# Kernel optimization log

Measured on AMD Instinct MI355X. Metric: run time of the kernel, lower is better.

Reference implementation:

```python
import jax, jax.numpy as jnp
import numpy as np

HEADS = 8
DIM_HEAD = 64
EPS = 1e-5  # nn.InstanceNorm1d default


def _inst_norm(t):
    # t: [b, h, n, d]; InstanceNorm1d(dim_head) on (b*h, n, d) input normalizes
    # over the last (L) axis per (instance, channel) = per (b, h, n) token.
    mu = jnp.mean(t, axis=-1, keepdims=True)
    var = jnp.var(t, axis=-1, keepdims=True)  # biased, matches torch eval-mode IN
    return (t - mu) / jnp.sqrt(var + EPS)


def setup_inputs() -> dict:
    key = jax.random.key(0)
    k1, k2, k3, k4 = jax.random.split(key, 4)
    b, n, dim = 4, 8192, 256
    inner = HEADS * DIM_HEAD  # 512
    x = jax.random.normal(k1, (b, n, dim), dtype=jnp.float32)
    w_qkv = jax.random.normal(k2, (dim, 3 * inner), dtype=jnp.float32) * (1.0 / DIM_HEAD)
    w_out = jax.random.normal(k3, (inner, dim), dtype=jnp.float32) * (dim ** -0.5)
    b_out = jax.random.normal(k4, (dim,), dtype=jnp.float32) * 0.01
    return {"x": x, "w_qkv": w_qkv, "w_out": w_out, "b_out": b_out}


def reference(x, w_qkv, w_out, b_out):
    b, n, dim = x.shape
    qkv = x @ w_qkv                                   # [b, n, 3*inner]
    q, k, v = jnp.split(qkv, 3, axis=-1)
    to_heads = lambda t: t.reshape(b, n, HEADS, DIM_HEAD).transpose(0, 2, 1, 3)  # b h n d
    q, k, v = to_heads(q), to_heads(k), to_heads(v)
    # Galerkin: instance-norm K and V
    k = _inst_norm(k)
    v = _inst_norm(v)
    # associative linear attention: (k^T v) then q @ dots, scaled by 1/n
    dots = jnp.einsum('bhnd,bhne->bhde', k, v)        # [b, h, d, d]
    out = jnp.einsum('bhnd,bhde->bhne', q, dots) * (1.0 / n)  # [b, h, n, d]
    out = out.transpose(0, 2, 1, 3).reshape(b, n, HEADS * DIM_HEAD)
    return out @ w_out + b_out                        # dropout p=0 (eval)
```

## Files before the change

kernel.cpp:

```cpp
#include <hip/hip_runtime.h>
#include <hip/hip_bf16.h>
#include <stdint.h>

#define HEADS 8
#define DHEAD 64
#define BATCH 4
#define SEQ   8192
#define DIM   256
#define INNER 512
#define QKVC  1536
#define ROWS  32768
#define EPS   1e-5f

typedef unsigned short u16;
typedef unsigned long long u64;
typedef __attribute__((ext_vector_type(8))) short bf16x8;
typedef __attribute__((ext_vector_type(4))) float f32x4;

#define AS1 __attribute__((address_space(1)))
#define AS3 __attribute__((address_space(3)))

__device__ __forceinline__ void async16(const void* g, void* l) {
  __builtin_amdgcn_global_load_lds((AS1 unsigned int*)g, (AS3 unsigned int*)l, 16, 0, 0);
}

__device__ __forceinline__ float bf2f(u16 u) {
  union { uint32_t i; float f; } v; v.i = ((uint32_t)u) << 16; return v.f;
}
__device__ __forceinline__ u16 f2bf(float f) {
  union { float f; uint32_t i; } v; v.f = f;
  uint32_t x = v.i;
  return (u16)((x + 0x7fffu + ((x >> 16) & 1u)) >> 16);
}

__global__ __launch_bounds__(256) void prep(const float* __restrict__ x,
                                            const float* __restrict__ w,
                                            u16* __restrict__ xb,
                                            u16* __restrict__ wqB,
                                            u16* __restrict__ wkvP,
                                            float* __restrict__ dots) {
  int bid = blockIdx.x;
  if (bid < 8192) {
    int i = (bid * 256 + threadIdx.x) * 4;
    float4 v = *(const float4*)(x + i);
    ushort4 o; o.x = f2bf(v.x); o.y = f2bf(v.y); o.z = f2bf(v.z); o.w = f2bf(v.w);
    *(ushort4*)(xb + i) = o;
  } else if (bid < 8704) {
    int id = (bid - 8192) * 256 + threadIdx.x;
    int k = id >> 9, j = id & 511;
    wqB[id] = f2bf(w[k * QKVC + j]);
  } else if (bid < 9728) {
    int id = (bid - 8704) * 256 + threadIdx.x;
    int j    = id & 7;
    int lane = (id >> 3) & 63;
    int frag = (id >> 9) & 63;
    int h    = id >> 15;
    int fn   = frag & 3;
    int half = (frag >> 2) & 1;
    int ks   = (frag >> 3) & 1;
    int kk   = frag >> 4;
    int col  = half * 64 + fn * 16 + (lane & 15);
    int kidx = kk * 64 + ks * 32 + (lane >> 4) * 8 + j;
    int oc   = (col < 64) ? (512 + h * 64 + col) : (1024 + h * 64 + (col - 64));
    wkvP[id] = f2bf(w[kidx * QKVC + oc]);
  } else {
    int i = ((bid - 9728) * 256 + threadIdx.x) * 4;
    float4 z; z.x = 0.f; z.y = 0.f; z.z = 0.f; z.w = 0.f;
    *(float4*)(dots + i) = z;
  }
}

__device__ __forceinline__ void gemm_tile(const u16* __restrict__ A, int lda,
                                          const u16* __restrict__ Bt, int ldb,
                                          int K, int row0, int col0,
                                          u16* sA, u16* sB, f32x4 acc[4][4]) {
  const int tid = threadIdx.x, lane = tid & 63, wave = tid >> 6;
  const int m = lane & 15, q = lane >> 4;
  const int mr = (wave >> 1) * 64, nc = (wave & 1) * 64;
  for (int kk = 0; kk < K; kk += 64) {
#pragma unroll
    for (int it = 0; it < 4; ++it) {
      int c = it * 256 + tid;
      int r = c >> 3, kc = (c ^ r) & 7;
      async16(A + (size_t)(row0 + r) * lda + kk + kc * 8, sA + (it * 256 + wave * 64) * 8);
      async16(Bt + (size_t)(col0 + r) * ldb + kk + kc * 8, sB + (it * 256 + wave * 64) * 8);
    }
    __syncthreads();
#pragma unroll
    for (int ks = 0; ks < 2; ++ks) {
      bf16x8 af[4], bfr[4];
#pragma unroll
      for (int f = 0; f < 4; ++f) {
        int ra = mr + f * 16 + m;
        int rb = nc + f * 16 + m;
        af[f]  = *(const bf16x8*)&sA[ra * 64 + (((ks * 4 + q) ^ (m & 7)) * 8)];
        bfr[f] = *(const bf16x8*)&sB[rb * 64 + (((ks * 4 + q) ^ (m & 7)) * 8)];
      }
#pragma unroll
      for (int fm = 0; fm < 4; ++fm)
#pragma unroll
        for (int fn = 0; fn < 4; ++fn)
          acc[fm][fn] = __builtin_amdgcn_mfma_f32_16x16x32_bf16(af[fm], bfr[fn], acc[fm][fn], 0, 0, 0);
    }
    __syncthreads();
  }
}

__global__ __launch_bounds__(256, 3) void gemm_kv_dots(const u16* __restrict__ A,
                                                       const u16* __restrict__ wkvP,
                                                       float* __restrict__ dots) {
  __shared__ alignas(16) u16 smem[17408];
  u16* sA  = smem;
  u16* knT = smem;
  u16* vnT = smem + 8704;

  const int tid = threadIdx.x, lane = tid & 63, wave = tid >> 6;
  const int m = lane & 15, q = lane >> 4;
  const int row0 = blockIdx.x * 128;
  const int h = blockIdx.y;
  const int half = wave & 1;
  const int rowbase = (wave >> 1) * 64;
  const u16* bp = wkvP + (size_t)h * 32768 + lane * 8;

  f32x4 acc[4][4];
#pragma unroll
  for (int i = 0; i < 4; ++i)
#pragma unroll
    for (int j = 0; j < 4; ++j) acc[i][j] = (f32x4){0.f, 0.f, 0.f, 0.f};

#pragma unroll
  for (int kk = 0; kk < 4; ++kk) {
    bf16x8 breg[2][4];
#pragma unroll
    for (int ks = 0; ks < 2; ++ks)
#pragma unroll
      for (int fn = 0; fn < 4; ++fn)
        breg[ks][fn] = *(const bf16x8*)(bp + (size_t)((((kk * 2 + ks) * 2 + half) * 4 + fn) * 512));
#pragma unroll
    for (int it = 0; it < 4; ++it) {
      int c = it * 256 + tid;
      int r = c >> 3, kc = (c ^ r) & 7;
      async16(A + (size_t)(row0 + r) * DIM + kk * 64 + kc * 8, sA + (it * 256 + wave * 64) * 8);
    }
    __syncthreads();
#pragma unroll
    for (int ks = 0; ks < 2; ++ks) {
      bf16x8 af[4];
#pragma unroll
      for (int f = 0; f < 4; ++f) {
        int r = rowbase + f * 16 + m;
        af[f] = *(const bf16x8*)&sA[r * 64 + (((ks * 4 + q) ^ (m & 7)) * 8)];
      }
#pragma unroll
      for (int fm = 0; fm < 4; ++fm)
#pragma unroll
        for (int fn = 0; fn < 4; ++fn)
          acc[fm][fn] = __builtin_amdgcn_mfma_f32_16x16x32_bf16(af[fm], breg[ks][fn], acc[fm][fn], 0, 0, 0);
    }
    __syncthreads();
  }

  u16* dst = half ? vnT : knT;
#pragma unroll
  for (int fm = 0; fm < 4; ++fm) {
    f32x4 s  = acc[fm][0] + acc[fm][1] + acc[fm][2] + acc[fm][3];
    f32x4 s2 = (f32x4){0.f, 0.f, 0.f, 0.f};
#pragma unroll
    for (int fn = 0; fn < 4; ++fn)
#pragma unroll
      for (int r = 0; r < 4; ++r) s2[r] = fmaf(acc[fm][fn][r], acc[fm][fn][r], s2[r]);
#pragma unroll
    for (int mask = 1; mask <= 8; mask <<= 1) {
#pragma unroll
      for (int r = 0; r < 4; ++r) {
        s[r]  += __shfl_xor(s[r],  mask, 64);
        s2[r] += __shfl_xor(s2[r], mask, 64);
      }
    }
    f32x4 mu, rs;
#pragma unroll
    for (int r = 0; r < 4; ++r) {
      mu[r] = s[r] * (1.f / 64.f);
      float var = s2[r] * (1.f / 64.f) - mu[r] * mu[r];
      rs[r] = rsqrtf(var + EPS);
    }
    const int tokb = rowbase + fm * 16 + q * 4;
#pragma unroll
    for (int fn = 0; fn < 4; ++fn) {
      int d = fn * 16 + m;
      u64 pk = 0;
#pragma unroll
      for (int r = 0; r < 4; ++r) {
        u16 hv = f2bf((acc[fm][fn][r] - mu[r]) * rs[r]);
        pk |= (u64)hv << (16 * r);
      }
      *(u64*)(dst + d * 136 + tokb) = pk;
    }
  }
  __syncthreads();

  f32x4 dacc[4];
#pragma unroll
  for (int f = 0; f < 4; ++f) dacc[f] = (f32x4){0.f, 0.f, 0.f, 0.f};
#pragma unroll
  for (int ks = 0; ks < 4; ++ks) {
    bf16x8 a = *(const bf16x8*)&knT[(wave * 16 + m) * 136 + ks * 32 + q * 8];
#pragma unroll
    for (int fn = 0; fn < 4; ++fn) {
      bf16x8 bb = *(const bf16x8*)&vnT[(fn * 16 + m) * 136 + ks * 32 + q * 8];
      dacc[fn] = __builtin_amdgcn_mfma_f32_16x16x32_bf16(a, bb, dacc[fn], 0, 0, 0);
    }
  }

  const int b = blockIdx.x >> 6;
  float* dbase = dots + (size_t)(b * 8 + h) * 4096;
#pragma unroll
  for (int fn = 0; fn < 4; ++fn) {
    int e = fn * 16 + m;
#pragma unroll
    for (int r = 0; r < 4; ++r) {
      int d = wave * 16 + q * 4 + r;
      atomicAdd(dbase + d * 64 + e, dacc[fn][r]);
    }
  }
}

__global__ __launch_bounds__(256) void make_M(const float* __restrict__ dots,
                                              const float* __restrict__ wout,
                                              u16* __restrict__ Mbt) {
  __shared__ float dl[8][64];
  const int bh = blockIdx.x, b = bh >> 3, h = bh & 7;
  const int jg = blockIdx.y;
  const int c = threadIdx.x;
  for (int i = threadIdx.x; i < 512; i += 256)
    ((float*)dl)[i] = dots[(size_t)bh * 4096 + jg * 512 + i];
  __syncthreads();
  float accv[8];
#pragma unroll
  for (int jj = 0; jj < 8; ++jj) accv[jj] = 0.f;
  for (int e = 0; e < 64; ++e) {
    float w = wout[(h * 64 + e) * DIM + c];
#pragma unroll
    for (int jj = 0; jj < 8; ++jj) accv[jj] = fmaf(dl[jj][e], w, accv[jj]);
  }
  const float inv_n = 1.0f / (float)SEQ;
  u16* outp = Mbt + ((size_t)(b * 256 + c)) * 512 + h * 64 + jg * 8;
#pragma unroll
  for (int jj = 0; jj < 8; ++jj) outp[jj] = f2bf(accv[jj] * inv_n);
}

__global__ __launch_bounds__(256) void make_G(const u16* __restrict__ Mbt,
                                              const u16* __restrict__ wqB,
                                              u16* __restrict__ Gt) {
  __shared__ alignas(16) u16 sA[128 * 64];
  __shared__ alignas(16) u16 sB[128 * 64];
  const int lane = threadIdx.x & 63, wave = threadIdx.x >> 6;
  const int row0 = blockIdx.x * 128, col0 = blockIdx.y * 128;
  const int b = blockIdx.z;
  f32x4 acc[4][4];
#pragma unroll
  for (int i = 0; i < 4; ++i)
#pragma unroll
    for (int j = 0; j < 4; ++j) acc[i][j] = (f32x4){0.f, 0.f, 0.f, 0.f};

  gemm_tile(Mbt + (size_t)b * 256 * 512, INNER, wqB, INNER, INNER, row0, col0, sA, sB, acc);

  u16* out = Gt + (size_t)b * 256 * 256;
  const int mr = (wave >> 1) * 64, nc = (wave & 1) * 64;
#pragma unroll
  for (int fm = 0; fm < 4; ++fm) {
    int rbase = row0 + mr + fm * 16 + (lane >> 4) * 4;
#pragma unroll
    for (int fn = 0; fn < 4; ++fn) {
      int col = col0 + nc + fn * 16 + (lane & 15);
#pragma unroll
      for (int r = 0; r < 4; ++r)
        out[(size_t)(rbase + r) * DIM + col] = f2bf(acc[fm][fn][r]);
    }
  }
}

__global__ __launch_bounds__(256) void gemm_out(const u16* __restrict__ A,
                                                const u16* __restrict__ Gt,
                                                const float* __restrict__ bias,
                                                float* __restrict__ out) {
  __shared__ alignas(16) u16 sA[128 * 64];
  __shared__ alignas(16) u16 sB[128 * 64];
  const int lane = threadIdx.x & 63, wave = threadIdx.x >> 6;
  const int row0 = blockIdx.x * 128, col0 = blockIdx.y * 128;
  const int b = blockIdx.x >> 6;
  const u16* Bt = Gt + (size_t)b * 256 * 256;
  f32x4 acc[4][4];
#pragma unroll
  for (int i = 0; i < 4; ++i)
#pragma unroll
    for (int j = 0; j < 4; ++j) acc[i][j] = (f32x4){0.f, 0.f, 0.f, 0.f};

  gemm_tile(A, DIM, Bt, DIM, DIM, row0, col0, sA, sB, acc);

  const int mr = (wave >> 1) * 64, nc = (wave & 1) * 64;
#pragma unroll
  for (int fm = 0; fm < 4; ++fm) {
    int rbase = row0 + mr + fm * 16 + (lane >> 4) * 4;
#pragma unroll
    for (int fn = 0; fn < 4; ++fn) {
      int col = col0 + nc + fn * 16 + (lane & 15);
      float bb = bias[col];
#pragma unroll
      for (int r = 0; r < 4; ++r)
        out[(size_t)(rbase + r) * DIM + col] = acc[fm][fn][r] + bb;
    }
  }
}

extern "C" void kernel_launch(void* const* d_in, const int* in_sizes, int n_in,
                              void* d_out, int out_size, void* d_ws, size_t ws_size,
                              hipStream_t stream) {
  const float* x     = (const float*)d_in[0];
  const float* w_qkv = (const float*)d_in[1];
  const float* w_out = (const float*)d_in[2];
  const float* b_out = (const float*)d_in[3];
  float* out = (float*)d_out;

  char* ws = (char*)d_ws;
  size_t off = 0;
  u16* xb    = (u16*)(ws + off); off += (size_t)ROWS * DIM * 2;
  u16* wqB   = (u16*)(ws + off); off += (size_t)DIM * INNER * 2;
  u16* wkvP  = (u16*)(ws + off); off += (size_t)HEADS * 128 * DIM * 2;
  float* dots = (float*)(ws + off); off += (size_t)32 * 64 * 64 * 4;
  u16* Mbt   = (u16*)(ws + off); off += (size_t)BATCH * 256 * 512 * 2;
  u16* Gt    = (u16*)(ws + off); off += (size_t)BATCH * 256 * 256 * 2;

  prep<<<9856, 256, 0, stream>>>(x, w_qkv, xb, wqB, wkvP, dots);
  gemm_kv_dots<<<dim3(ROWS / 128, HEADS), 256, 0, stream>>>(xb, wkvP, dots);
  make_M<<<dim3(32, 8), 256, 0, stream>>>(dots, w_out, Mbt);
  make_G<<<dim3(2, 2, BATCH), 256, 0, stream>>>(Mbt, wqB, Gt);
  gemm_out<<<dim3(ROWS / 128, 2), 256, 0, stream>>>(xb, Gt, b_out, out);
}
```

Measured before the change: 174.2 us.

## Stage full A tile once in LDS and process two heads per block

gemm_kv_dots now loads the full 128x256 bf16 x tile into LDS in one async batch and computes two heads per block. This halves the grid and the repeated reads of x, and drops the per-k-step syncs. gemm_out likewise stages the full A tile once and reads B fragments straight from global memory, skipping LDS staging for B. The trade is a larger LDS footprint (64KB) with fewer blocks per CU and doubled accumulator registers, which may limit occupancy and latency hiding.

New measurement: 187.7 us. +7.7%, slower.

```diff
diff --git a/kernel.cpp b/kernel.cpp
--- a/kernel.cpp
+++ b/kernel.cpp
@@ -106,121 +106,137 @@
   }
 }
 
-__global__ __launch_bounds__(256, 3) void gemm_kv_dots(const u16* __restrict__ A,
+__global__ __launch_bounds__(256, 2) void gemm_kv_dots(const u16* __restrict__ A,
                                                        const u16* __restrict__ wkvP,
                                                        float* __restrict__ dots) {
-  __shared__ alignas(16) u16 smem[17408];
-  u16* sA  = smem;
-  u16* knT = smem;
-  u16* vnT = smem + 8704;
-
+  __shared__ alignas(16) u16 smem[32768];
   const int tid = threadIdx.x, lane = tid & 63, wave = tid >> 6;
   const int m = lane & 15, q = lane >> 4;
   const int row0 = blockIdx.x * 128;
-  const int h = blockIdx.y;
+  const int hp = blockIdx.y;
   const int half = wave & 1;
   const int rowbase = (wave >> 1) * 64;
-  const u16* bp = wkvP + (size_t)h * 32768 + lane * 8;
-
-  f32x4 acc[4][4];
+  const u16* bpA = wkvP + (size_t)(2 * hp) * 32768 + lane * 8;
+  const u16* bpB = wkvP + (size_t)(2 * hp + 1) * 32768 + lane * 8;
+
+#pragma unroll
+  for (int it = 0; it < 16; ++it) {
+    int c = it * 256 + tid;
+    int r = c >> 5, kc = (c ^ r) & 31;
+    async16(A + (size_t)(row0 + r) * DIM + kc * 8, smem + c * 8);
+  }
+
+  f32x4 acc[4][8];
 #pragma unroll
   for (int i = 0; i < 4; ++i)
 #pragma unroll
-    for (int j = 0; j < 4; ++j) acc[i][j] = (f32x4){0.f, 0.f, 0.f, 0.f};
-
-#pragma unroll
+    for (int j = 0; j < 8; ++j) acc[i][j] = (f32x4){0.f, 0.f, 0.f, 0.f};
+
+  __syncthreads();
+
   for (int kk = 0; kk < 4; ++kk) {
-    bf16x8 breg[2][4];
-#pragma unroll
-    for (int ks = 0; ks < 2; ++ks)
+#pragma unroll
+    for (int ks = 0; ks < 2; ++ks) {
+      int fb = ((kk * 2 + ks) * 2 + half) * 4;
+      bf16x8 bra[4], brb[4];
+#pragma unroll
+      for (int fn = 0; fn < 4; ++fn) {
+        bra[fn] = *(const bf16x8*)(bpA + (size_t)(fb + fn) * 512);
+        brb[fn] = *(const bf16x8*)(bpB + (size_t)(fb + fn) * 512);
+      }
+      bf16x8 af[4];
+      int g = kk * 8 + ks * 4 + q;
+#pragma unroll
+      for (int f = 0; f < 4; ++f) {
+        int ra = rowbase + f * 16 + m;
+        af[f] = *(const bf16x8*)&smem[ra * 256 + ((g ^ (ra & 31)) * 8)];
+      }
+#pragma unroll
+      for (int fm = 0; fm < 4; ++fm)
+#pragma unroll
+        for (int fn = 0; fn < 4; ++fn) {
+          acc[fm][fn]     = __builtin_amdgcn_mfma_f32_16x16x32_bf16(af[fm], bra[fn], acc[fm][fn], 0, 0, 0);
+          acc[fm][4 + fn] = __builtin_amdgcn_mfma_f32_16x16x32_bf16(af[fm], brb[fn], acc[fm][4 + fn], 0, 0, 0);
+        }
+    }
+  }
+  __syncthreads();
+
+#pragma unroll
+  for (int h2 = 0; h2 < 2; ++h2) {
+    u16* matb = smem + h2 * 16384 + (half ? 8192 : 0);
+#pragma unroll
+    for (int fm = 0; fm < 4; ++fm) {
+      f32x4 s  = acc[fm][h2 * 4 + 0] + acc[fm][h2 * 4 + 1] + acc[fm][h2 * 4 + 2] + acc[fm][h2 * 4 + 3];
+      f32x4 s2 = (f32x4){0.f, 0.f, 0.f, 0.f};
 #pragma unroll
       for (int fn = 0; fn < 4; ++fn)
-        breg[ks][fn] = *(const bf16x8*)(bp + (size_t)((((kk * 2 + ks) * 2 + half) * 4 + fn) * 512));
-#pragma unroll
-    for (int it = 0; it < 4; ++it) {
-      int c = it * 256 + tid;
-      int r = c >> 3, kc = (c ^ r) & 7;
-      async16(A + (size_t)(row0 + r) * DIM + kk * 64 + kc * 8, sA + (it * 256 + wave * 64) * 8);
-    }
-    __syncthreads();
-#pragma unroll
-    for (int ks = 0; ks < 2; ++ks) {
-      bf16x8 af[4];
-#pragma unroll
-      for (int f = 0; f < 4; ++f) {
-        int r = rowbase + f * 16 + m;
-        af[f] = *(const bf16x8*)&sA[r * 64 + (((ks * 4 + q) ^ (m & 7)) * 8)];
-      }
-#pragma unroll
-      for (int fm = 0; fm < 4; ++fm)
-#pragma unroll
-        for (int fn = 0; fn < 4; ++fn)
-          acc[fm][fn] = __builtin_amdgcn_mfma_f32_16x16x32_bf16(af[fm], breg[ks][fn], acc[fm][fn], 0, 0, 0);
-    }
-    __syncthreads();
-  }
-
-  u16* dst = half ? vnT : knT;
-#pragma unroll
-  for (int fm = 0; fm < 4; ++fm) {
-    f32x4 s  = acc[fm][0] + acc[fm][1] + acc[fm][2] + acc[fm][3];
-    f32x4 s2 = (f32x4){0.f, 0.f, 0.f, 0.f};
-#pragma unroll
-    for (int fn = 0; fn < 4; ++fn)
-#pragma unroll
-      for (int r = 0; r < 4; ++r) s2[r] = fmaf(acc[fm][fn][r], acc[fm][fn][r], s2[r]);
-#pragma unroll
-    for (int mask = 1; mask <= 8; mask <<= 1) {
+#pragma unroll
+        for (int r = 0; r < 4; ++r) {
+          float a = acc[fm][h2 * 4 + fn][r];
+          s2[r] = fmaf(a, a, s2[r]);
+        }
+#pragma unroll
+      for (int mask = 1; mask <= 8; mask <<= 1) {
+#pragma unroll
+        for (int r = 0; r < 4; ++r) {
+          s[r]  += __shfl_xor(s[r],  mask, 64);
+          s2[r] += __shfl_xor(s2[r], mask, 64);
+        }
+      }
+      f32x4 mu, rs;
 #pragma unroll
       for (int r = 0; r < 4; ++r) {
-        s[r]  += __shfl_xor(s[r],  mask, 64);
-        s2[r] += __shfl_xor(s2[r], mask, 64);
-      }
-    }
-    f32x4 mu, rs;
-#pragma unroll
-    for (int r = 0; r < 4; ++r) {
-      mu[r] = s[r] * (1.f / 64.f);
-      float var = s2[r] * (1.f / 64.f) - mu[r] * mu[r];
-      rs[r] = rsqrtf(var + EPS);
-    }
-    const int tokb = rowbase + fm * 16 + q * 4;
+        mu[r] = s[r] * (1.f / 64.f);
+        float var = s2[r] * (1.f / 64.f) - mu[r] * mu[r];
+        rs[r] = rsqrtf(var + EPS);
+      }
+      const int c8 = (rowbase >> 2) + fm * 4 + q;
+#pragma unroll
+      for (int fn = 0; fn < 4; ++fn) {
+        int d = fn * 16 + m;
+        u64 pk = 0;
+#pragma unroll
+        for (int r = 0; r < 4; ++r) {
+          u16 hv = f2bf((acc[fm][h2 * 4 + fn][r] - mu[r]) * rs[r]);
+          pk |= (u64)hv << (16 * r);
+        }
+        int slot8 = (((c8 >> 1) ^ (d & 15)) << 1) | (c8 & 1);
+        *(u64*)(matb + d * 128 + slot8 * 4) = pk;
+      }
+    }
+  }
+  __syncthreads();
+
+  const int b = blockIdx.x >> 6;
+#pragma unroll
+  for (int h2 = 0; h2 < 2; ++h2) {
+    const u16* kn = smem + h2 * 16384;
+    const u16* vn = kn + 8192;
+    f32x4 dacc[4];
+#pragma unroll
+    for (int f = 0; f < 4; ++f) dacc[f] = (f32x4){0.f, 0.f, 0.f, 0.f};
+#pragma unroll
+    for (int ks = 0; ks < 4; ++ks) {
+      int c16 = ks * 4 + q;
+      int da = wave * 16 + m;
+      bf16x8 a = *(const bf16x8*)&kn[da * 128 + ((c16 ^ (da & 15)) * 8)];
+#pragma unroll
+      for (int fn = 0; fn < 4; ++fn) {
+        int e = fn * 16 + m;
+        bf16x8 bb = *(const bf16x8*)&vn[e * 128 + ((c16 ^ (e & 15)) * 8)];
+        dacc[fn] = __builtin_amdgcn_mfma_f32_16x16x32_bf16(a, bb, dacc[fn], 0, 0, 0);
+      }
+    }
+    float* dbase = dots + (size_t)(b * 8 + hp * 2 + h2) * 4096;
 #pragma unroll
     for (int fn = 0; fn < 4; ++fn) {
-      int d = fn * 16 + m;
-      u64 pk = 0;
+      int e = fn * 16 + m;
 #pragma unroll
       for (int r = 0; r < 4; ++r) {
-        u16 hv = f2bf((acc[fm][fn][r] - mu[r]) * rs[r]);
-        pk |= (u64)hv << (16 * r);
-      }
-      *(u64*)(dst + d * 136 + tokb) = pk;
-    }
-  }
-  __syncthreads();
-
-  f32x4 dacc[4];
-#pragma unroll
-  for (int f = 0; f < 4; ++f) dacc[f] = (f32x4){0.f, 0.f, 0.f, 0.f};
-#pragma unroll
-  for (int ks = 0; ks < 4; ++ks) {
-    bf16x8 a = *(const bf16x8*)&knT[(wave * 16 + m) * 136 + ks * 32 + q * 8];
-#pragma unroll
-    for (int fn = 0; fn < 4; ++fn) {
-      bf16x8 bb = *(const bf16x8*)&vnT[(fn * 16 + m) * 136 + ks * 32 + q * 8];
-      dacc[fn] = __builtin_amdgcn_mfma_f32_16x16x32_bf16(a, bb, dacc[fn], 0, 0, 0);
-    }
-  }
-
-  const int b = blockIdx.x >> 6;
-  float* dbase = dots + (size_t)(b * 8 + h) * 4096;
-#pragma unroll
-  for (int fn = 0; fn < 4; ++fn) {
-    int e = fn * 16 + m;
-#pragma unroll
-    for (int r = 0; r < 4; ++r) {
-      int d = wave * 16 + q * 4 + r;
-      atomicAdd(dbase + d * 64 + e, dacc[fn][r]);
+        int d = wave * 16 + q * 4 + r;
+        atomicAdd(dbase + d * 64 + e, dacc[fn][r]);
+      }
     }
   }
 }
@@ -280,31 +296,61 @@
   }
 }
 
-__global__ __launch_bounds__(256) void gemm_out(const u16* __restrict__ A,
-                                                const u16* __restrict__ Gt,
-                                                const float* __restrict__ bias,
-                                                float* __restrict__ out) {
-  __shared__ alignas(16) u16 sA[128 * 64];
-  __shared__ alignas(16) u16 sB[128 * 64];
-  const int lane = threadIdx.x & 63, wave = threadIdx.x >> 6;
+__global__ __launch_bounds__(256, 2) void gemm_out(const u16* __restrict__ A,
+                                                   const u16* __restrict__ Gt,
+                                                   const float* __restrict__ bias,
+                                                   float* __restrict__ out) {
+  __shared__ alignas(16) u16 smem[32768];
+  const int tid = threadIdx.x, lane = tid & 63, wave = tid >> 6;
+  const int m = lane & 15, q = lane >> 4;
   const int row0 = blockIdx.x * 128, col0 = blockIdx.y * 128;
   const int b = blockIdx.x >> 6;
   const u16* Bt = Gt + (size_t)b * 256 * 256;
+  const int mr = (wave >> 1) * 64, nc = (wave & 1) * 64;
+
+#pragma unroll
+  for (int it = 0; it < 16; ++it) {
+    int c = it * 256 + tid;
+    int r = c >> 5, kc = (c ^ r) & 31;
+    async16(A + (size_t)(row0 + r) * DIM + kc * 8, smem + c * 8);
+  }
+
   f32x4 acc[4][4];
 #pragma unroll
   for (int i = 0; i < 4; ++i)
 #pragma unroll
     for (int j = 0; j < 4; ++j) acc[i][j] = (f32x4){0.f, 0.f, 0.f, 0.f};
 
-  gemm_tile(A, DIM, Bt, DIM, DIM, row0, col0, sA, sB, acc);
-
-  const int mr = (wave >> 1) * 64, nc = (wave & 1) * 64;
+  __syncthreads();
+
+  for (int kk = 0; kk < 4; ++kk) {
+#pragma unroll
+    for (int ks = 0; ks < 2; ++ks) {
+      bf16x8 bfr[4];
+#pragma unroll
+      for (int fn = 0; fn < 4; ++fn)
+        bfr[fn] = *(const bf16x8*)(Bt + (size_t)(col0 + nc + fn * 16 + m) * 256 + kk * 64 + ks * 32 + q * 8);
+      bf16x8 af[4];
+      int g = kk * 8 + ks * 4 + q;
+#pragma unroll
+      for (int f = 0; f < 4; ++f) {
+        int ra = mr + f * 16 + m;
+        af[f] = *(const bf16x8*)&smem[ra * 256 + ((g ^ (ra & 31)) * 8)];
+      }
+#pragma unroll
+      for (int fm = 0; fm < 4; ++fm)
+#pragma unroll
+        for (int fn = 0; fn < 4; ++fn)
+          acc[fm][fn] = __builtin_amdgcn_mfma_f32_16x16x32_bf16(af[fm], bfr[fn], acc[fm][fn], 0, 0, 0);
+    }
+  }
+
 #pragma unroll
   for (int fm = 0; fm < 4; ++fm) {
-    int rbase = row0 + mr + fm * 16 + (lane >> 4) * 4;
+    int rbase = row0 + mr + fm * 16 + q * 4;
 #pragma unroll
     for (int fn = 0; fn < 4; ++fn) {
-      int col = col0 + nc + fn * 16 + (lane & 15);
+      int col = col0 + nc + fn * 16 + m;
       float bb = bias[col];
 #pragma unroll
       for (int r = 0; r < 4; ++r)
@@ -332,7 +378,7 @@
   u16* Gt    = (u16*)(ws + off); off += (size_t)BATCH * 256 * 256 * 2;
 
   prep<<<9856, 256, 0, stream>>>(x, w_qkv, xb, wqB, wkvP, dots);
-  gemm_kv_dots<<<dim3(ROWS / 128, HEADS), 256, 0, stream>>>(xb, wkvP, dots);
+  gemm_kv_dots<<<dim3(ROWS / 128, HEADS / 2), 256, 0, stream>>>(xb, wkvP, dots);
   make_M<<<dim3(32, 8), 256, 0, stream>>>(dots, w_out, Mbt);
   make_G<<<dim3(2, 2, BATCH), 256, 0, stream>>>(Mbt, wqB, Gt);
   gemm_out<<<dim3(ROWS / 128, 2), 256, 0, stream>>>(xb, Gt, b_out, out);
```

## Loop gemm_kv_dots over four row tiles and stage full A tile in gemm_out

Applied to the files above, without the earlier changes.

gemm_kv_dots now processes four 128-row tiles per block and keeps the k^T v accumulator in registers across them. This cuts grid size and the number of float atomicAdds to dots by a factor of four. gemm_out now loads the whole 128x256 A tile into LDS with one async burst and reads B fragments straight from global memory, instead of running the double-staged gemm_tile loop. The costs are a longer serial chain per block, fewer blocks in flight, and uncoalesced global B loads inside the inner loop.

Result: slower. 178.9 us (+2.7%).

```diff
diff --git a/kernel.cpp b/kernel.cpp
--- a/kernel.cpp
+++ b/kernel.cpp
@@ -106,7 +106,7 @@
   }
 }
 
-__global__ __launch_bounds__(256, 3) void gemm_kv_dots(const u16* __restrict__ A,
+__global__ __launch_bounds__(256, 2) void gemm_kv_dots(const u16* __restrict__ A,
                                                        const u16* __restrict__ wkvP,
                                                        float* __restrict__ dots) {
   __shared__ alignas(16) u16 smem[17408];
@@ -116,103 +116,108 @@
 
   const int tid = threadIdx.x, lane = tid & 63, wave = tid >> 6;
   const int m = lane & 15, q = lane >> 4;
-  const int row0 = blockIdx.x * 128;
   const int h = blockIdx.y;
   const int half = wave & 1;
   const int rowbase = (wave >> 1) * 64;
   const u16* bp = wkvP + (size_t)h * 32768 + lane * 8;
 
-  f32x4 acc[4][4];
-#pragma unroll
-  for (int i = 0; i < 4; ++i)
-#pragma unroll
-    for (int j = 0; j < 4; ++j) acc[i][j] = (f32x4){0.f, 0.f, 0.f, 0.f};
-
-#pragma unroll
-  for (int kk = 0; kk < 4; ++kk) {
-    bf16x8 breg[2][4];
-#pragma unroll
-    for (int ks = 0; ks < 2; ++ks)
+  f32x4 dacc[4];
+#pragma unroll
+  for (int f = 0; f < 4; ++f) dacc[f] = (f32x4){0.f, 0.f, 0.f, 0.f};
+
+  for (int t = 0; t < 4; ++t) {
+    const int row0 = (blockIdx.x * 4 + t) * 128;
+
+    f32x4 acc[4][4];
+#pragma unroll
+    for (int i = 0; i < 4; ++i)
+#pragma unroll
+      for (int j = 0; j < 4; ++j) acc[i][j] = (f32x4){0.f, 0.f, 0.f, 0.f};
+
+#pragma unroll
+    for (int kk = 0; kk < 4; ++kk) {
+      bf16x8 breg[2][4];
+#pragma unroll
+      for (int ks = 0; ks < 2; ++ks)
+#pragma unroll
+        for (int fn = 0; fn < 4; ++fn)
+          breg[ks][fn] = *(const bf16x8*)(bp + (size_t)((((kk * 2 + ks) * 2 + half) * 4 + fn) * 512));
+#pragma unroll
+      for (int it = 0; it < 4; ++it) {
+        int c = it * 256 + tid;
+        int r = c >> 3, kc = (c ^ r) & 7;
+        async16(A + (size_t)(row0 + r) * DIM + kk * 64 + kc * 8, sA + (it * 256 + wave * 64) * 8);
+      }
+      __syncthreads();
+#pragma unroll
+      for (int ks = 0; ks < 2; ++ks) {
+        bf16x8 af[4];
+#pragma unroll
+        for (int f = 0; f < 4; ++f) {
+          int r = rowbase + f * 16 + m;
+          af[f] = *(const bf16x8*)&sA[r * 64 + (((ks * 4 + q) ^ (m & 7)) * 8)];
+        }
+#pragma unroll
+        for (int fm = 0; fm < 4; ++fm)
+#pragma unroll
+          for (int fn = 0; fn < 4; ++fn)
+            acc[fm][fn] = __builtin_amdgcn_mfma_f32_16x16x32_bf16(af[fm], breg[ks][fn], acc[fm][fn], 0, 0, 0);
+      }
+      __syncthreads();
+    }
+
+    u16* dst = half ? vnT : knT;
+#pragma unroll
+    for (int fm = 0; fm < 4; ++fm) {
+      f32x4 s  = acc[fm][0] + acc[fm][1] + acc[fm][2] + acc[fm][3];
+      f32x4 s2 = (f32x4){0.f, 0.f, 0.f, 0.f};
 #pragma unroll
       for (int fn = 0; fn < 4; ++fn)
-        breg[ks][fn] = *(const bf16x8*)(bp + (size_t)((((kk * 2 + ks) * 2 + half) * 4 + fn) * 512));
-#pragma unroll
-    for (int it = 0; it < 4; ++it) {
-      int c = it * 256 + tid;
-      int r = c >> 3, kc = (c ^ r) & 7;
-      async16(A + (size_t)(row0 + r) * DIM + kk * 64 + kc * 8, sA + (it * 256 + wave * 64) * 8);
+#pragma unroll
+        for (int r = 0; r < 4; ++r) s2[r] = fmaf(acc[fm][fn][r], acc[fm][fn][r], s2[r]);
+#pragma unroll
+      for (int mask = 1; mask <= 8; mask <<= 1) {
+#pragma unroll
+        for (int r = 0; r < 4; ++r) {
+          s[r]  += __shfl_xor(s[r],  mask, 64);
+          s2[r] += __shfl_xor(s2[r], mask, 64);
+        }
+      }
+      f32x4 mu, rs;
+#pragma unroll
+      for (int r = 0; r < 4; ++r) {
+        mu[r] = s[r] * (1.f / 64.f);
+        float var = s2[r] * (1.f / 64.f) - mu[r] * mu[r];
+        rs[r] = rsqrtf(var + EPS);
+      }
+      const int tokb = rowbase + fm * 16 + q * 4;
+#pragma unroll
+      for (int fn = 0; fn < 4; ++fn) {
+        int d = fn * 16 + m;
+        u64 pk = 0;
+#pragma unroll
+        for (int r = 0; r < 4; ++r) {
+          u16 hv = f2bf((acc[fm][fn][r] - mu[r]) * rs[r]);
+          pk |= (u64)hv << (16 * r);
+        }
+        *(u64*)(dst + d * 136 + tokb) = pk;
+      }
     }
     __syncthreads();
-#pragma unroll
-    for (int ks = 0; ks < 2; ++ks) {
-      bf16x8 af[4];
-#pragma unroll
-      for (int f = 0; f < 4; ++f) {
-        int r = rowbase + f * 16 + m;
-        af[f] = *(const bf16x8*)&sA[r * 64 + (((ks * 4 + q) ^ (m & 7)) * 8)];
-      }
-#pragma unroll
-      for (int fm = 0; fm < 4; ++fm)
-#pragma unroll
-        for (int fn = 0; fn < 4; ++fn)
-          acc[fm][fn] = __builtin_amdgcn_mfma_f32_16x16x32_bf16(af[fm], breg[ks][fn], acc[fm][fn], 0, 0, 0);
+
+#pragma unroll
+    for (int ks = 0; ks < 4; ++ks) {
+      bf16x8 a = *(const bf16x8*)&knT[(wave * 16 + m) * 136 + ks * 32 + q * 8];
+#pragma unroll
+      for (int fn = 0; fn < 4; ++fn) {
+        bf16x8 bb = *(const bf16x8*)&vnT[(fn * 16 + m) * 136 + ks * 32 + q * 8];
+        dacc[fn] = __builtin_amdgcn_mfma_f32_16x16x32_bf16(a, bb, dacc[fn], 0, 0, 0);
+      }
     }
     __syncthreads();
   }
 
-  u16* dst = half ? vnT : knT;
-#pragma unroll
-  for (int fm = 0; fm < 4; ++fm) {
-    f32x4 s  = acc[fm][0] + acc[fm][1] + acc[fm][2] + acc[fm][3];
-    f32x4 s2 = (f32x4){0.f, 0.f, 0.f, 0.f};
-#pragma unroll
-    for (int fn = 0; fn < 4; ++fn)
-#pragma unroll
-      for (int r = 0; r < 4; ++r) s2[r] = fmaf(acc[fm][fn][r], acc[fm][fn][r], s2[r]);
-#pragma unroll
-    for (int mask = 1; mask <= 8; mask <<= 1) {
-#pragma unroll
-      for (int r = 0; r < 4; ++r) {
-        s[r]  += __shfl_xor(s[r],  mask, 64);
-        s2[r] += __shfl_xor(s2[r], mask, 64);
-      }
-    }
-    f32x4 mu, rs;
-#pragma unroll
-    for (int r = 0; r < 4; ++r) {
-      mu[r] = s[r] * (1.f / 64.f);
-      float var = s2[r] * (1.f / 64.f) - mu[r] * mu[r];
-      rs[r] = rsqrtf(var + EPS);
-    }
-    const int tokb = rowbase + fm * 16 + q * 4;
-#pragma unroll
-    for (int fn = 0; fn < 4; ++fn) {
-      int d = fn * 16 + m;
-      u64 pk = 0;
-#pragma unroll
-      for (int r = 0; r < 4; ++r) {
-        u16 hv = f2bf((acc[fm][fn][r] - mu[r]) * rs[r]);
-        pk |= (u64)hv << (16 * r);
-      }
-      *(u64*)(dst + d * 136 + tokb) = pk;
-    }
-  }
-  __syncthreads();
-
-  f32x4 dacc[4];
-#pragma unroll
-  for (int f = 0; f < 4; ++f) dacc[f] = (f32x4){0.f, 0.f, 0.f, 0.f};
-#pragma unroll
-  for (int ks = 0; ks < 4; ++ks) {
-    bf16x8 a = *(const bf16x8*)&knT[(wave * 16 + m) * 136 + ks * 32 + q * 8];
-#pragma unroll
-    for (int fn = 0; fn < 4; ++fn) {
-      bf16x8 bb = *(const bf16x8*)&vnT[(fn * 16 + m) * 136 + ks * 32 + q * 8];
-      dacc[fn] = __builtin_amdgcn_mfma_f32_16x16x32_bf16(a, bb, dacc[fn], 0, 0, 0);
-    }
-  }
-
-  const int b = blockIdx.x >> 6;
+  const int b = blockIdx.x >> 4;
   float* dbase = dots + (size_t)(b * 8 + h) * 4096;
 #pragma unroll
   for (int fn = 0; fn < 4; ++fn) {
@@ -280,31 +285,61 @@
   }
 }
 
-__global__ __launch_bounds__(256) void gemm_out(const u16* __restrict__ A,
-                                                const u16* __restrict__ Gt,
-                                                const float* __restrict__ bias,
-                                                float* __restrict__ out) {
-  __shared__ alignas(16) u16 sA[128 * 64];
-  __shared__ alignas(16) u16 sB[128 * 64];
-  const int lane = threadIdx.x & 63, wave = threadIdx.x >> 6;
+__global__ __launch_bounds__(256, 2) void gemm_out(const u16* __restrict__ A,
+                                                   const u16* __restrict__ Gt,
+                                                   const float* __restrict__ bias,
+                                                   float* __restrict__ out) {
+  __shared__ alignas(16) u16 smem[32768];
+  const int tid = threadIdx.x, lane = tid & 63, wave = tid >> 6;
+  const int m = lane & 15, q = lane >> 4;
   const int row0 = blockIdx.x * 128, col0 = blockIdx.y * 128;
   const int b = blockIdx.x >> 6;
   const u16* Bt = Gt + (size_t)b * 256 * 256;
+  const int mr = (wave >> 1) * 64, nc = (wave & 1) * 64;
+
+#pragma unroll
+  for (int it = 0; it < 16; ++it) {
+    int c = it * 256 + tid;
+    int r = c >> 5, kc = (c ^ r) & 31;
+    async16(A + (size_t)(row0 + r) * DIM + kc * 8, smem + c * 8);
+  }
+
   f32x4 acc[4][4];
 #pragma unroll
   for (int i = 0; i < 4; ++i)
 #pragma unroll
     for (int j = 0; j < 4; ++j) acc[i][j] = (f32x4){0.f, 0.f, 0.f, 0.f};
 
-  gemm_tile(A, DIM, Bt, DIM, DIM, row0, col0, sA, sB, acc);
-
-  const int mr = (wave >> 1) * 64, nc = (wave & 1) * 64;
+  __syncthreads();
+
+  for (int kk = 0; kk < 4; ++kk) {
+#pragma unroll
+    for (int ks = 0; ks < 2; ++ks) {
+      bf16x8 bfr[4];
+#pragma unroll
+      for (int fn = 0; fn < 4; ++fn)
+        bfr[fn] = *(const bf16x8*)(Bt + (size_t)(col0 + nc + fn * 16 + m) * 256 + kk * 64 + ks * 32 + q * 8);
+      bf16x8 af[4];
+      int g = kk * 8 + ks * 4 + q;
+#pragma unroll
+      for (int f = 0; f < 4; ++f) {
+        int ra = mr + f * 16 + m;
+        af[f] = *(const bf16x8*)&smem[ra * 256 + ((g ^ (ra & 31)) * 8)];
+      }
+#pragma unroll
+      for (int fm = 0; fm < 4; ++fm)
+#pragma unroll
+        for (int fn = 0; fn < 4; ++fn)
+          acc[fm][fn] = __builtin_amdgcn_mfma_f32_16x16x32_bf16(af[fm], bfr[fn], acc[fm][fn], 0, 0, 0);
+    }
+  }
+
 #pragma unroll
   for (int fm = 0; fm < 4; ++fm) {
-    int rbase = row0 + mr + fm * 16 + (lane >> 4) * 4;
+    int rbase = row0 + mr + fm * 16 + q * 4;
 #pragma unroll
     for (int fn = 0; fn < 4; ++fn) {
-      int col = col0 + nc + fn * 16 + (lane & 15);
+      int col = col0 + nc + fn * 16 + m;
       float bb = bias[col];
 #pragma unroll
       for (int r = 0; r < 4; ++r)
@@ -332,7 +367,7 @@
   u16* Gt    = (u16*)(ws + off); off += (size_t)BATCH * 256 * 256 * 2;
 
   prep<<<9856, 256, 0, stream>>>(x, w_qkv, xb, wqB, wkvP, dots);
-  gemm_kv_dots<<<dim3(ROWS / 128, HEADS), 256, 0, stream>>>(xb, wkvP, dots);
+  gemm_kv_dots<<<dim3(ROWS / 512, HEADS), 256, 0, stream>>>(xb, wkvP, dots);
   make_M<<<dim3(32, 8), 256, 0, stream>>>(dots, w_out, Mbt);
   make_G<<<dim3(2, 2, BATCH), 256, 0, stream>>>(Mbt, wqB, Gt);
   gemm_out<<<dim3(ROWS / 128, 2), 256, 0, stream>>>(xb, Gt, b_out, out);
```

## Load GEMM operands directly from global memory and process two row tiles per block

Applied to the files above, without the earlier changes.

Both gemm_kv_dots and gemm_out now read A (and B in gemm_out) fragments straight from global memory into registers, dropping the async LDS staging and its barriers. gemm_kv_dots also handles two 128-row tiles per block, accumulating dots across them so there are half as many blocks and half as many atomicAdds into dots. Launch bounds change to 2 blocks per SM. This trades shared-memory staging and sync overhead for uncoalesced strided global reads that rely on the cache, plus higher register pressure.

Result: slower. 189.5 us (+8.8%).

```diff
diff --git a/kernel.cpp b/kernel.cpp
--- a/kernel.cpp
+++ b/kernel.cpp
@@ -106,113 +106,103 @@
   }
 }
 
-__global__ __launch_bounds__(256, 3) void gemm_kv_dots(const u16* __restrict__ A,
+__global__ __launch_bounds__(256, 2) void gemm_kv_dots(const u16* __restrict__ A,
                                                        const u16* __restrict__ wkvP,
                                                        float* __restrict__ dots) {
   __shared__ alignas(16) u16 smem[17408];
-  u16* sA  = smem;
   u16* knT = smem;
   u16* vnT = smem + 8704;
 
   const int tid = threadIdx.x, lane = tid & 63, wave = tid >> 6;
   const int m = lane & 15, q = lane >> 4;
-  const int row0 = blockIdx.x * 128;
   const int h = blockIdx.y;
   const int half = wave & 1;
   const int rowbase = (wave >> 1) * 64;
   const u16* bp = wkvP + (size_t)h * 32768 + lane * 8;
 
-  f32x4 acc[4][4];
-#pragma unroll
-  for (int i = 0; i < 4; ++i)
-#pragma unroll
-    for (int j = 0; j < 4; ++j) acc[i][j] = (f32x4){0.f, 0.f, 0.f, 0.f};
-
-#pragma unroll
-  for (int kk = 0; kk < 4; ++kk) {
-    bf16x8 breg[2][4];
-#pragma unroll
-    for (int ks = 0; ks < 2; ++ks)
+  f32x4 dacc[4];
+#pragma unroll
+  for (int f = 0; f < 4; ++f) dacc[f] = (f32x4){0.f, 0.f, 0.f, 0.f};
+
+  for (int t = 0; t < 2; ++t) {
+    const int row0 = (blockIdx.x * 2 + t) * 128;
+    const u16* ab = A + (size_t)(row0 + rowbase + m) * DIM + q * 8;
+
+    f32x4 acc[4][4];
+#pragma unroll
+    for (int i = 0; i < 4; ++i)
+#pragma unroll
+      for (int j = 0; j < 4; ++j) acc[i][j] = (f32x4){0.f, 0.f, 0.f, 0.f};
+
+#pragma unroll
+    for (int kx = 0; kx < 8; ++kx) {
+      const int fb = (kx * 2 + half) * 4;
+      bf16x8 bfr[4], af[4];
 #pragma unroll
       for (int fn = 0; fn < 4; ++fn)
-        breg[ks][fn] = *(const bf16x8*)(bp + (size_t)((((kk * 2 + ks) * 2 + half) * 4 + fn) * 512));
-#pragma unroll
-    for (int it = 0; it < 4; ++it) {
-      int c = it * 256 + tid;
-      int r = c >> 3, kc = (c ^ r) & 7;
-      async16(A + (size_t)(row0 + r) * DIM + kk * 64 + kc * 8, sA + (it * 256 + wave * 64) * 8);
+        bfr[fn] = *(const bf16x8*)(bp + (size_t)(fb + fn) * 512);
+#pragma unroll
+      for (int f = 0; f < 4; ++f)
+        af[f] = *(const bf16x8*)(ab + (size_t)(f * 16) * DIM + kx * 32);
+#pragma unroll
+      for (int fm = 0; fm < 4; ++fm)
+#pragma unroll
+        for (int fn = 0; fn < 4; ++fn)
+          acc[fm][fn] = __builtin_amdgcn_mfma_f32_16x16x32_bf16(af[fm], bfr[fn], acc[fm][fn], 0, 0, 0);
+    }
+
+    u16* dst = half ? vnT : knT;
+#pragma unroll
+    for (int fm = 0; fm < 4; ++fm) {
+      f32x4 s  = acc[fm][0] + acc[fm][1] + acc[fm][2] + acc[fm][3];
+      f32x4 s2 = (f32x4){0.f, 0.f, 0.f, 0.f};
+#pragma unroll
+      for (int fn = 0; fn < 4; ++fn)
+#pragma unroll
+        for (int r = 0; r < 4; ++r) s2[r] = fmaf(acc[fm][fn][r], acc[fm][fn][r], s2[r]);
+#pragma unroll
+      for (int mask = 1; mask <= 8; mask <<= 1) {
+#pragma unroll
+        for (int r = 0; r < 4; ++r) {
+          s[r]  += __shfl_xor(s[r],  mask, 64);
+          s2[r] += __shfl_xor(s2[r], mask, 64);
+        }
+      }
+      f32x4 mu, rs;
+#pragma unroll
+      for (int r = 0; r < 4; ++r) {
+        mu[r] = s[r] * (1.f / 64.f);
+        float var = s2[r] * (1.f / 64.f) - mu[r] * mu[r];
+        rs[r] = rsqrtf(var + EPS);
+      }
+      const int tokb = rowbase + fm * 16 + q * 4;
+#pragma unroll
+      for (int fn = 0; fn < 4; ++fn) {
+        int d = fn * 16 + m;
+        u64 pk = 0;
+#pragma unroll
+        for (int r = 0; r < 4; ++r) {
+          u16 hv = f2bf((acc[fm][fn][r] - mu[r]) * rs[r]);
+          pk |= (u64)hv << (16 * r);
+        }
+        *(u64*)(dst + d * 136 + tokb) = pk;
+      }
     }
     __syncthreads();
-#pragma unroll
-    for (int ks = 0; ks < 2; ++ks) {
-      bf16x8 af[4];
-#pragma unroll
-      for (int f = 0; f < 4; ++f) {
-        int r = rowbase + f * 16 + m;
-        af[f] = *(const bf16x8*)&sA[r * 64 + (((ks * 4 + q) ^ (m & 7)) * 8)];
-      }
-#pragma unroll
-      for (int fm = 0; fm < 4; ++fm)
-#pragma unroll
-        for (int fn = 0; fn < 4; ++fn)
-          acc[fm][fn] = __builtin_amdgcn_mfma_f32_16x16x32_bf16(af[fm], breg[ks][fn], acc[fm][fn], 0, 0, 0);
+
+#pragma unroll
+    for (int ks = 0; ks < 4; ++ks) {
+      bf16x8 a = *(const bf16x8*)&knT[(wave * 16 + m) * 136 + ks * 32 + q * 8];
+#pragma unroll
+      for (int fn = 0; fn < 4; ++fn) {
+        bf16x8 bb = *(const bf16x8*)&vnT[(fn * 16 + m) * 136 + ks * 32 + q * 8];
+        dacc[fn] = __builtin_amdgcn_mfma_f32_16x16x32_bf16(a, bb, dacc[fn], 0, 0, 0);
+      }
     }
     __syncthreads();
   }
 
-  u16* dst = half ? vnT : knT;
-#pragma unroll
-  for (int fm = 0; fm < 4; ++fm) {
-    f32x4 s  = acc[fm][0] + acc[fm][1] + acc[fm][2] + acc[fm][3];
-    f32x4 s2 = (f32x4){0.f, 0.f, 0.f, 0.f};
-#pragma unroll
-    for (int fn = 0; fn < 4; ++fn)
-#pragma unroll
-      for (int r = 0; r < 4; ++r) s2[r] = fmaf(acc[fm][fn][r], acc[fm][fn][r], s2[r]);
-#pragma unroll
-    for (int mask = 1; mask <= 8; mask <<= 1) {
-#pragma unroll
-      for (int r = 0; r < 4; ++r) {
-        s[r]  += __shfl_xor(s[r],  mask, 64);
-        s2[r] += __shfl_xor(s2[r], mask, 64);
-      }
-    }
-    f32x4 mu, rs;
-#pragma unroll
-    for (int r = 0; r < 4; ++r) {
-      mu[r] = s[r] * (1.f / 64.f);
-      float var = s2[r] * (1.f / 64.f) - mu[r] * mu[r];
-      rs[r] = rsqrtf(var + EPS);
-    }
-    const int tokb = rowbase + fm * 16 + q * 4;
-#pragma unroll
-    for (int fn = 0; fn < 4; ++fn) {
-      int d = fn * 16 + m;
-      u64 pk = 0;
-#pragma unroll
-      for (int r = 0; r < 4; ++r) {
-        u16 hv = f2bf((acc[fm][fn][r] - mu[r]) * rs[r]);
-        pk |= (u64)hv << (16 * r);
-      }
-      *(u64*)(dst + d * 136 + tokb) = pk;
-    }
-  }
-  __syncthreads();
-
-  f32x4 dacc[4];
-#pragma unroll
-  for (int f = 0; f < 4; ++f) dacc[f] = (f32x4){0.f, 0.f, 0.f, 0.f};
-#pragma unroll
-  for (int ks = 0; ks < 4; ++ks) {
-    bf16x8 a = *(const bf16x8*)&knT[(wave * 16 + m) * 136 + ks * 32 + q * 8];
-#pragma unroll
-    for (int fn = 0; fn < 4; ++fn) {
-      bf16x8 bb = *(const bf16x8*)&vnT[(fn * 16 + m) * 136 + ks * 32 + q * 8];
-      dacc[fn] = __builtin_amdgcn_mfma_f32_16x16x32_bf16(a, bb, dacc[fn], 0, 0, 0);
-    }
-  }
-
-  const int b = blockIdx.x >> 6;
+  const int b = blockIdx.x >> 5;
   float* dbase = dots + (size_t)(b * 8 + h) * 4096;
 #pragma unroll
   for (int fn = 0; fn < 4; ++fn) {
@@ -280,35 +270,51 @@
   }
 }
 
-__global__ __launch_bounds__(256) void gemm_out(const u16* __restrict__ A,
-                                                const u16* __restrict__ Gt,
-                                                const float* __restrict__ bias,
-                                                float* __restrict__ out) {
-  __shared__ alignas(16) u16 sA[128 * 64];
-  __shared__ alignas(16) u16 sB[128 * 64];
-  const int lane = threadIdx.x & 63, wave = threadIdx.x >> 6;
+__global__ __launch_bounds__(256, 2) void gemm_out(const u16* __restrict__ A,
+                                                   const u16* __restrict__ Gt,
+                                                   const float* __restrict__ bias,
+                                                   float* __restrict__ out) {
+  const int tid = threadIdx.x, lane = tid & 63, wave = tid >> 6;
+  const int m = lane & 15, q = lane >> 4;
   const int row0 = blockIdx.x * 128, col0 = blockIdx.y * 128;
   const int b = blockIdx.x >> 6;
   const u16* Bt = Gt + (size_t)b * 256 * 256;
+  const int mr = (wave >> 1) * 64, nc = (wave & 1) * 64;
+  const u16* ab = A  + (size_t)(row0 + mr + m) * DIM + q * 8;
+  const u16* bb = Bt + (size_t)(col0 + nc + m) * DIM + q * 8;
+
   f32x4 acc[4][4];
 #pragma unroll
   for (int i = 0; i < 4; ++i)
 #pragma unroll
     for (int j = 0; j < 4; ++j) acc[i][j] = (f32x4){0.f, 0.f, 0.f, 0.f};
 
-  gemm_tile(A, DIM, Bt, DIM, DIM, row0, col0, sA, sB, acc);
-
-  const int mr = (wave >> 1) * 64, nc = (wave & 1) * 64;
+#pragma unroll
+  for (int kx = 0; kx < 8; ++kx) {
+    bf16x8 af[4], bfr[4];
+#pragma unroll
+    for (int f = 0; f < 4; ++f)
+      af[f]  = *(const bf16x8*)(ab + (size_t)(f * 16) * DIM + kx * 32);
+#pragma unroll
+    for (int fn = 0; fn < 4; ++fn)
+      bfr[fn] = *(const bf16x8*)(bb + (size_t)(fn * 16) * DIM + kx * 32);
+#pragma unroll
+    for (int fm = 0; fm < 4; ++fm)
+#pragma unroll
+      for (int fn = 0; fn < 4; ++fn)
+        acc[fm][fn] = __builtin_amdgcn_mfma_f32_16x16x32_bf16(af[fm], bfr[fn], acc[fm][fn], 0, 0, 0);
+  }
+
 #pragma unroll
   for (int fm = 0; fm < 4; ++fm) {
-    int rbase = row0 + mr + fm * 16 + (lane >> 4) * 4;
+    int rbase = row0 + mr + fm * 16 + q * 4;
 #pragma unroll
     for (int fn = 0; fn < 4; ++fn) {
-      int col = col0 + nc + fn * 16 + (lane & 15);
-      float bb = bias[col];
+      int col = col0 + nc + fn * 16 + m;
+      float bb2 = bias[col];
 #pragma unroll
       for (int r = 0; r < 4; ++r)
-        out[(size_t)(rbase + r) * DIM + col] = acc[fm][fn][r] + bb;
+        out[(size_t)(rbase + r) * DIM + col] = acc[fm][fn][r] + bb2;
     }
   }
 }
@@ -332,7 +338,7 @@
   u16* Gt    = (u16*)(ws + off); off += (size_t)BATCH * 256 * 256 * 2;
 
   prep<<<9856, 256, 0, stream>>>(x, w_qkv, xb, wqB, wkvP, dots);
-  gemm_kv_dots<<<dim3(ROWS / 128, HEADS), 256, 0, stream>>>(xb, wkvP, dots);
+  gemm_kv_dots<<<dim3(ROWS / 256, HEADS), 256, 0, stream>>>(xb, wkvP, dots);
   make_M<<<dim3(32, 8), 256, 0, stream>>>(dots, w_out, Mbt);
   make_G<<<dim3(2, 2, BATCH), 256, 0, stream>>>(Mbt, wqB, Gt);
   gemm_out<<<dim3(ROWS / 128, 2), 256, 0, stream>>>(xb, Gt, b_out, out);
```
